# Performance work log

Hardware: AMD Instinct MI355X
Metric: run time of the kernel (lower is better)

Reference implementation:

```python
import jax, jax.numpy as jnp
import numpy as np

N_NODES = 100000
N_EDGES = 1600000
D_IN = 64
D_HID = 64
D_OUT = 64


def _sage_conv(x, src, dst, n_nodes, W_l, b_l, W_r):
    # mean aggregation of source features at destination nodes
    msgs = x[src]  # [E, F] gather
    agg = jax.ops.segment_sum(msgs, dst, num_segments=n_nodes)
    cnt = jax.ops.segment_sum(jnp.ones((src.shape[0],), x.dtype), dst, num_segments=n_nodes)
    mean = agg / jnp.maximum(cnt, 1.0)[:, None]  # nodes with no in-edges -> 0
    # out = lin_l(mean) + lin_r(x); lin_l has bias, lin_r does not (PyG default)
    return mean @ W_l.T + b_l + x @ W_r.T


def setup_inputs() -> dict:
    key = jax.random.key(0)
    ks = jax.random.split(key, 8)
    x = jax.random.normal(ks[0], (N_NODES, D_IN), dtype=jnp.float32)
    edge_index = jax.random.randint(ks[1], (2, N_EDGES), 0, N_NODES, dtype=jnp.int64) if jax.config.jax_enable_x64 else jax.random.randint(ks[1], (2, N_EDGES), 0, N_NODES, dtype=jnp.int32)
    s1 = 1.0 / np.sqrt(D_IN)
    s2 = 1.0 / np.sqrt(D_HID)
    W1_l = jax.random.uniform(ks[2], (D_HID, D_IN), jnp.float32, -s1, s1)
    b1_l = jax.random.uniform(ks[3], (D_HID,), jnp.float32, -s1, s1)
    W1_r = jax.random.uniform(ks[4], (D_HID, D_IN), jnp.float32, -s1, s1)
    W2_l = jax.random.uniform(ks[5], (D_OUT, D_HID), jnp.float32, -s2, s2)
    b2_l = jax.random.uniform(ks[6], (D_OUT,), jnp.float32, -s2, s2)
    W2_r = jax.random.uniform(ks[7], (D_OUT, D_HID), jnp.float32, -s2, s2)
    return {"x": x, "edge_index": edge_index, "W1_l": W1_l, "b1_l": b1_l, "W1_r": W1_r,
            "W2_l": W2_l, "b2_l": b2_l, "W2_r": W2_r}


def reference(x, edge_index, W1_l, b1_l, W1_r, W2_l, b2_l, W2_r):
    src, dst = edge_index[0], edge_index[1]
    h = _sage_conv(x, src, dst, x.shape[0], W1_l, b1_l, W1_r)
    h = jax.nn.relu(h)
    out = _sage_conv(h, src, dst, x.shape[0], W2_l, b2_l, W2_r)
    return out
```

## Files before the change

kernel.cpp:

```cpp
#include <hip/hip_runtime.h>
#include <hip/hip_fp16.h>

#define N_NODES 100000
#define N_EDGES 1600000
#define D 64

#define BSHIFT 7
#define BUCK_N 128
#define NBUCK 782
#define EPB 4096
#define NBLKA 391
#define SCAN_N (NBUCK * NBLKA)
#define SCAN_B1 ((SCAN_N + 255) / 256)
#define A4_CAP 3072
#define X_OCTETS (N_NODES * D / 8)
#define CVT_BLKS ((X_OCTETS + 2048 + 511) / 512)
#define AGB (N_NODES / 32)

typedef _Float16 half8 __attribute__((ext_vector_type(8)));
typedef float floatx4 __attribute__((ext_vector_type(4)));


__device__ __forceinline__ uint4 pack8h(float4 a, float4 b) {
    __half2 h0, h1, h2, h3;
    h0.x = __float2half(a.x); h0.y = __float2half(a.y);
    h1.x = __float2half(a.z); h1.y = __float2half(a.w);
    h2.x = __float2half(b.x); h2.y = __float2half(b.y);
    h3.x = __float2half(b.z); h3.y = __float2half(b.w);
    uint4 pk;
    pk.x = *(unsigned int*)&h0; pk.y = *(unsigned int*)&h1;
    pk.z = *(unsigned int*)&h2; pk.w = *(unsigned int*)&h3;
    return pk;
}


__global__ void pre_k(const float* __restrict__ x,
                      const float* __restrict__ W1l, const float* __restrict__ W1r,
                      const float* __restrict__ W2l, const float* __restrict__ W2r,
                      const int* __restrict__ dst, int* __restrict__ histG,
                      __half* __restrict__ x16,
                      __half* __restrict__ o1l, __half* __restrict__ o1r,
                      __half* __restrict__ o2l, __half* __restrict__ o2r) {
    __shared__ int hl[1024];
    int t = threadIdx.x;
    if (blockIdx.x < NBLKA) {
        hl[t] = 0; hl[t + 512] = 0;
        __syncthreads();
        int base = blockIdx.x * EPB;
#pragma unroll
        for (int r = 0; r < 8; r++) {
            int idx = base + r * 512 + t;
            if (idx < N_EDGES) atomicAdd(&hl[dst[idx] >> BSHIFT], 1);
        }
        __syncthreads();
        histG[t * NBLKA + blockIdx.x] = hl[t];
        int u = t + 512;
        if (u < NBUCK) histG[u * NBLKA + blockIdx.x] = hl[u];
        return;
    }
    int i = (blockIdx.x - NBLKA) * 512 + t;
    const float* s;
    __half* d;
    int j;
    if (i < X_OCTETS) {
        s = x; d = x16; j = i * 8;
    } else {
        int k = i - X_OCTETS;
        if (k >= 2048) return;
        int arr = k >> 9;
        j = (k & 511) * 8;
        s = (arr == 0) ? W1l : (arr == 1) ? W1r : (arr == 2) ? W2l : W2r;
        d = (arr == 0) ? o1l : (arr == 1) ? o1r : (arr == 2) ? o2l : o2r;
    }
    float4 a = *(const float4*)&s[j];
    float4 b = *(const float4*)&s[j + 4];
    *(uint4*)&d[j] = pack8h(a, b);
}


__global__ void scan1_k(int* __restrict__ data, int* __restrict__ bsums, int n) {
    __shared__ int sm[256];
    int i = blockIdx.x * 256 + threadIdx.x;
    int v = (i < n) ? data[i] : 0;
    sm[threadIdx.x] = v;
    __syncthreads();
    for (int off = 1; off < 256; off <<= 1) {
        int t = (threadIdx.x >= off) ? sm[threadIdx.x - off] : 0;
        __syncthreads();
        sm[threadIdx.x] += t;
        __syncthreads();
    }
    if (i < n) data[i] = sm[threadIdx.x] - v;
    if (threadIdx.x == 255) bsums[blockIdx.x] = sm[255];
}

__global__ void scan2_k(int* __restrict__ bsums, int nb) {
    __shared__ int sm[1024];
    int t = threadIdx.x;
    int i0 = 2 * t, i1 = 2 * t + 1;
    int v0 = (i0 < nb) ? bsums[i0] : 0;
    int v1 = (i1 < nb) ? bsums[i1] : 0;
    int p = v0 + v1;
    sm[t] = p;
    __syncthreads();
    for (int off = 1; off < 1024; off <<= 1) {
        int tt = (t >= off) ? sm[t - off] : 0;
        __syncthreads();
        sm[t] += tt;
        __syncthreads();
    }
    int S = sm[t];
    if (i0 < nb) bsums[i0] = S - v1;
    if (i1 < nb) bsums[i1] = S;
}

__device__ __forceinline__ int hist_abs(const int* histG, const int* bsums, int idx) {
    int v = histG[idx];
    int blk = idx >> 8;
    if (blk > 0) v += bsums[blk - 1];
    return v;
}


__global__ void a3_sort_k(const int* __restrict__ src, const int* __restrict__ dst,
                          const int* __restrict__ histG, const int* __restrict__ bsums,
                          unsigned int* __restrict__ epacked, int e) {
    __shared__ int hl[1024];
    __shared__ int cur[1024];
    __shared__ int sc[512];
    __shared__ int gbase[NBUCK];
    __shared__ unsigned int spk[EPB];
    __shared__ unsigned short sb[EPB];
    int t = threadIdx.x;
    int blk = blockIdx.x;
    int base = blk * EPB;

    hl[t] = 0; hl[t + 512] = 0;
    __syncthreads();

    int myd[8], mys[8];
#pragma unroll
    for (int r = 0; r < 8; r++) {
        int idx = base + r * 512 + t;
        if (idx < e) {
            myd[r] = dst[idx];
            mys[r] = src[idx];
            atomicAdd(&hl[myd[r] >> BSHIFT], 1);
        } else {
            myd[r] = -1; mys[r] = 0;
        }
    }
    __syncthreads();

    int v0 = hl[2 * t], v1 = hl[2 * t + 1];
    int p = v0 + v1;
    sc[t] = p;
    __syncthreads();
    for (int off = 1; off < 512; off <<= 1) {
        int tt = (t >= off) ? sc[t - off] : 0;
        __syncthreads();
        sc[t] += tt;
        __syncthreads();
    }
    int E = sc[t] - p;
    hl[2 * t] = E;       cur[2 * t] = E;
    hl[2 * t + 1] = E + v0; cur[2 * t + 1] = E + v0;
    if (t < NBUCK) gbase[t] = hist_abs(histG, bsums, t * NBLKA + blk);
    if (t + 512 < NBUCK) gbase[t + 512] = hist_abs(histG, bsums, (t + 512) * NBLKA + blk);
    __syncthreads();

#pragma unroll
    for (int r = 0; r < 8; r++) {
        if (myd[r] >= 0) {
            int b = myd[r] >> BSHIFT;
            int dl = myd[r] & (BUCK_N - 1);
            int pos = atomicAdd(&cur[b], 1);
            spk[pos] = ((unsigned)dl << 17) | (unsigned)mys[r];
            sb[pos] = (unsigned short)b;
        }
    }
    __syncthreads();

    int cnt = e - base; if (cnt > EPB) cnt = EPB;
#pragma unroll
    for (int r = 0; r < 8; r++) {
        int i = r * 512 + t;
        if (i < cnt) {
            int b = sb[i];
            epacked[gbase[b] + (i - hl[b])] = spk[i];
        }
    }
}


__global__ void a4_nodesort_k(unsigned int* __restrict__ epk,
                              const int* __restrict__ histG, const int* __restrict__ bsums,
                              int* __restrict__ row_ptr) {
    __shared__ int sorted[A4_CAP];
    __shared__ int hist[BUCK_N];
    __shared__ int cur[BUCK_N];
    __shared__ int sc[256];
    int b = blockIdx.x;
    int t = threadIdx.x;

    int s0 = hist_abs(histG, bsums, b * NBLKA);
    int s1 = (b == NBUCK - 1) ? N_EDGES : hist_abs(histG, bsums, (b + 1) * NBLKA);
    int cnt = s1 - s0;
    if (cnt > A4_CAP) cnt = A4_CAP;

    if (t < BUCK_N) hist[t] = 0;
    __syncthreads();

    unsigned int my[12];
    int mycnt = 0;
    for (int i = t; i < cnt; i += 256) {
        unsigned int p = epk[s0 + i];
        my[mycnt++] = p;
        atomicAdd(&hist[p >> 17], 1);
    }
    __syncthreads();

    int v = (t < BUCK_N) ? hist[t] : 0;
    sc[t] = v;
    __syncthreads();
    for (int off = 1; off < 256; off <<= 1) {
        int tt = (t >= off) ? sc[t - off] : 0;
        __syncthreads();
        sc[t] += tt;
        __syncthreads();
    }
    int start = sc[t] - v;
    if (t < BUCK_N) cur[t] = start;
    __syncthreads();

    for (int i = 0; i < mycnt; i++) {
        unsigned int p = my[i];
        int pos = atomicAdd(&cur[p >> 17], 1);
        sorted[pos] = (int)(p & 0x1FFFF);
    }
    __syncthreads();

    for (int i = t; i < cnt; i += 256) epk[s0 + i] = (unsigned int)sorted[i];

    if (t < BUCK_N) {
        int g = b * BUCK_N + t;
        if (g < N_NODES) row_ptr[g] = s0 + start;
    }
    if (b == NBUCK - 1 && t == 0) row_ptr[N_NODES] = N_EDGES;
}


__device__ __forceinline__ void addp(__half2* a, uint4 v) {
    const __half2* h = (const __half2*)&v;
    a[0] = __hadd2(a[0], h[0]);
    a[1] = __hadd2(a[1], h[1]);
    a[2] = __hadd2(a[2], h[2]);
    a[3] = __hadd2(a[3], h[3]);
}

__global__ void agg_gemm_k(const __half* __restrict__ feat16,
                           const int* __restrict__ row_ptr,
                           const int* __restrict__ adj,
                           const __half* __restrict__ Wl16,
                           const __half* __restrict__ Wr16,
                           const float* __restrict__ bl,
                           float* __restrict__ out32,
                           __half* __restrict__ out16,
                           int do_relu) {
    __shared__ __half mt[32 * 64];
    int t = threadIdx.x;
    int lane = t & 63;
    int w = t >> 6;
    int fp = lane & 7;
    int gl = lane & 56;
    int nloc = w * 8 + (lane >> 3);
    int node = blockIdx.x * 32 + nloc;
    const uint4* f16 = (const uint4*)feat16;

    int fcol = lane & 15;
    int quad = lane >> 4;
    int f = w * 16 + fcol;
    half8 b0 = *(const half8*)(Wl16 + (size_t)f * 64 + quad * 8);
    half8 b1 = *(const half8*)(Wl16 + (size_t)f * 64 + 32 + quad * 8);
    half8 b2 = *(const half8*)(Wr16 + (size_t)f * 64 + quad * 8);
    half8 b3 = *(const half8*)(Wr16 + (size_t)f * 64 + 32 + quad * 8);
    float bias = bl[f];

    int beg = row_ptr[node];
    int end = row_ptr[node + 1];
    __half2 z; z.x = __float2half(0.f); z.y = z.x;
    __half2 aA[4] = {z, z, z, z};
    __half2 aB[4] = {z, z, z, z};

    int e = beg;
    for (; e + 7 < end; e += 8) {
        int am = adj[e + fp];
        int n0 = __shfl(am, gl + 0);
        int n1 = __shfl(am, gl + 1);
        int n2 = __shfl(am, gl + 2);
        int n3 = __shfl(am, gl + 3);
        int n4 = __shfl(am, gl + 4);
        int n5 = __shfl(am, gl + 5);
        int n6 = __shfl(am, gl + 6);
        int n7 = __shfl(am, gl + 7);
        uint4 v0 = f16[(size_t)n0 * 8 + fp];
        uint4 v1 = f16[(size_t)n1 * 8 + fp];
        uint4 v2 = f16[(size_t)n2 * 8 + fp];
        uint4 v3 = f16[(size_t)n3 * 8 + fp];
        uint4 v4 = f16[(size_t)n4 * 8 + fp];
        uint4 v5 = f16[(size_t)n5 * 8 + fp];
        uint4 v6 = f16[(size_t)n6 * 8 + fp];
        uint4 v7 = f16[(size_t)n7 * 8 + fp];
        addp(aA, v0); addp(aB, v1); addp(aA, v2); addp(aB, v3);
        addp(aA, v4); addp(aB, v5); addp(aA, v6); addp(aB, v7);
    }
    if (e + 3 < end) {
        uint4 v0 = f16[(size_t)adj[e] * 8 + fp];
        uint4 v1 = f16[(size_t)adj[e + 1] * 8 + fp];
        uint4 v2 = f16[(size_t)adj[e + 2] * 8 + fp];
        uint4 v3 = f16[(size_t)adj[e + 3] * 8 + fp];
        addp(aA, v0); addp(aB, v1); addp(aA, v2); addp(aB, v3);
        e += 4;
    }
    for (; e < end; e++) addp(aA, f16[(size_t)adj[e] * 8 + fp]);

    int dg = end - beg;
    float inv = (dg > 1) ? 1.0f / (float)dg : 1.0f;
    float2 s0 = __half22float2(aA[0]), s1 = __half22float2(aA[1]);
    float2 s2 = __half22float2(aA[2]), s3 = __half22float2(aA[3]);
    float2 t0 = __half22float2(aB[0]), t1 = __half22float2(aB[1]);
    float2 t2 = __half22float2(aB[2]), t3 = __half22float2(aB[3]);
    float4 o0, o1;
    o0.x = (s0.x + t0.x) * inv; o0.y = (s0.y + t0.y) * inv;
    o0.z = (s1.x + t1.x) * inv; o0.w = (s1.y + t1.y) * inv;
    o1.x = (s2.x + t2.x) * inv; o1.y = (s2.y + t2.y) * inv;
    o1.z = (s3.x + t3.x) * inv; o1.w = (s3.y + t3.y) * inv;
    *(uint4*)&mt[(size_t)nloc * 64 + 8 * (fp ^ (nloc & 7))] = pack8h(o0, o1);
    __syncthreads();

#pragma unroll
    for (int tile = 0; tile < 2; tile++) {
        int row = tile * 16 + fcol;
        half8 a0 = *(const half8*)&mt[(size_t)row * 64 + 8 * (quad ^ (row & 7))];
        half8 a1 = *(const half8*)&mt[(size_t)row * 64 + 8 * ((4 + quad) ^ (row & 7))];
        size_t frow = ((size_t)blockIdx.x * 32 + row) * 64 + quad * 8;
        half8 a2 = *(const half8*)(feat16 + frow);
        half8 a3 = *(const half8*)(feat16 + frow + 32);

        floatx4 acc = {0.f, 0.f, 0.f, 0.f};
        acc = __builtin_amdgcn_mfma_f32_16x16x32_f16(a0, b0, acc, 0, 0, 0);
        acc = __builtin_amdgcn_mfma_f32_16x16x32_f16(a1, b1, acc, 0, 0, 0);
        acc = __builtin_amdgcn_mfma_f32_16x16x32_f16(a2, b2, acc, 0, 0, 0);
        acc = __builtin_amdgcn_mfma_f32_16x16x32_f16(a3, b3, acc, 0, 0, 0);

#pragma unroll
        for (int r = 0; r < 4; r++) {
            int node2 = blockIdx.x * 32 + tile * 16 + quad * 4 + r;
            float v = acc[r] + bias;
            if (do_relu) v = fmaxf(v, 0.f);
            if (out32) out32[(size_t)node2 * 64 + f] = v;
            if (out16) out16[(size_t)node2 * 64 + f] = __float2half(v);
        }
    }
}

extern "C" void kernel_launch(void* const* d_in, const int* in_sizes, int n_in,
                              void* d_out, int out_size, void* d_ws, size_t ws_size,
                              hipStream_t stream) {
    const float* x   = (const float*)d_in[0];
    const int*   ei  = (const int*)d_in[1];
    const float* W1l = (const float*)d_in[2];
    const float* b1l = (const float*)d_in[3];
    const float* W1r = (const float*)d_in[4];
    const float* W2l = (const float*)d_in[5];
    const float* b2l = (const float*)d_in[6];
    const float* W2r = (const float*)d_in[7];
    float* out = (float*)d_out;

    const int* src = ei;
    const int* dst = ei + N_EDGES;

    __half* x16   = (__half*)d_ws;
    __half* h16   = x16 + (size_t)N_NODES * D;
    __half* w1l16 = h16 + (size_t)N_NODES * D;
    __half* w1r16 = w1l16 + 4096;
    __half* w2l16 = w1r16 + 4096;
    __half* w2r16 = w2l16 + 4096;
    int*   histG = (int*)(w2r16 + 4096);
    int*   bsums = histG + SCAN_N;
    int*   row_ptr = bsums + 2048;
    unsigned int* epk = (unsigned int*)(row_ptr + N_NODES + 2);

    pre_k<<<NBLKA + CVT_BLKS, 512, 0, stream>>>(x, W1l, W1r, W2l, W2r, dst, histG,
                                                x16, w1l16, w1r16, w2l16, w2r16);

    scan1_k<<<SCAN_B1, 256, 0, stream>>>(histG, bsums, SCAN_N);
    scan2_k<<<1, 1024, 0, stream>>>(bsums, SCAN_B1);

    a3_sort_k<<<NBLKA, 512, 0, stream>>>(src, dst, histG, bsums, epk, N_EDGES);
    a4_nodesort_k<<<NBUCK, 256, 0, stream>>>(epk, histG, bsums, row_ptr);

    agg_gemm_k<<<AGB, 256, 0, stream>>>(x16, row_ptr, (const int*)epk,
                                        w1l16, w1r16, b1l,
                                        (float*)nullptr, h16, 1);
    agg_gemm_k<<<AGB, 256, 0, stream>>>(h16, row_ptr, (const int*)epk,
                                        w2l16, w2r16, b2l,
                                        out, (__half*)nullptr, 0);
}
```

Before: 199.6 us.

## Replace histogram+scan bucketing with atomic slot reservation into fixed-capacity buckets

Measured after the change: 201.2 us. About the same (+0.8%).

```diff
diff --git a/kernel.cpp b/kernel.cpp
--- a/kernel.cpp
+++ b/kernel.cpp
@@ -10,8 +10,6 @@
 #define NBUCK 782
 #define EPB 4096
 #define NBLKA 391
-#define SCAN_N (NBUCK * NBLKA)
-#define SCAN_B1 ((SCAN_N + 255) / 256)
 #define A4_CAP 3072
 #define X_OCTETS (N_NODES * D / 8)
 #define CVT_BLKS ((X_OCTETS + 2048 + 511) / 512)
@@ -34,106 +32,44 @@
 }
 
 
-__global__ void pre_k(const float* __restrict__ x,
-                      const float* __restrict__ W1l, const float* __restrict__ W1r,
-                      const float* __restrict__ W2l, const float* __restrict__ W2r,
-                      const int* __restrict__ dst, int* __restrict__ histG,
-                      __half* __restrict__ x16,
-                      __half* __restrict__ o1l, __half* __restrict__ o1r,
-                      __half* __restrict__ o2l, __half* __restrict__ o2r) {
-    __shared__ int hl[1024];
-    int t = threadIdx.x;
-    if (blockIdx.x < NBLKA) {
-        hl[t] = 0; hl[t + 512] = 0;
-        __syncthreads();
-        int base = blockIdx.x * EPB;
-#pragma unroll
-        for (int r = 0; r < 8; r++) {
-            int idx = base + r * 512 + t;
-            if (idx < N_EDGES) atomicAdd(&hl[dst[idx] >> BSHIFT], 1);
-        }
-        __syncthreads();
-        histG[t * NBLKA + blockIdx.x] = hl[t];
-        int u = t + 512;
-        if (u < NBUCK) histG[u * NBLKA + blockIdx.x] = hl[u];
-        return;
-    }
-    int i = (blockIdx.x - NBLKA) * 512 + t;
-    const float* s;
-    __half* d;
-    int j;
-    if (i < X_OCTETS) {
-        s = x; d = x16; j = i * 8;
-    } else {
-        int k = i - X_OCTETS;
-        if (k >= 2048) return;
-        int arr = k >> 9;
-        j = (k & 511) * 8;
-        s = (arr == 0) ? W1l : (arr == 1) ? W1r : (arr == 2) ? W2l : W2r;
-        d = (arr == 0) ? o1l : (arr == 1) ? o1r : (arr == 2) ? o2l : o2r;
-    }
-    float4 a = *(const float4*)&s[j];
-    float4 b = *(const float4*)&s[j + 4];
-    *(uint4*)&d[j] = pack8h(a, b);
-}
-
-
-__global__ void scan1_k(int* __restrict__ data, int* __restrict__ bsums, int n) {
-    __shared__ int sm[256];
-    int i = blockIdx.x * 256 + threadIdx.x;
-    int v = (i < n) ? data[i] : 0;
-    sm[threadIdx.x] = v;
-    __syncthreads();
-    for (int off = 1; off < 256; off <<= 1) {
-        int t = (threadIdx.x >= off) ? sm[threadIdx.x - off] : 0;
-        __syncthreads();
-        sm[threadIdx.x] += t;
-        __syncthreads();
-    }
-    if (i < n) data[i] = sm[threadIdx.x] - v;
-    if (threadIdx.x == 255) bsums[blockIdx.x] = sm[255];
-}
-
-__global__ void scan2_k(int* __restrict__ bsums, int nb) {
-    __shared__ int sm[1024];
-    int t = threadIdx.x;
-    int i0 = 2 * t, i1 = 2 * t + 1;
-    int v0 = (i0 < nb) ? bsums[i0] : 0;
-    int v1 = (i1 < nb) ? bsums[i1] : 0;
-    int p = v0 + v1;
-    sm[t] = p;
-    __syncthreads();
-    for (int off = 1; off < 1024; off <<= 1) {
-        int tt = (t >= off) ? sm[t - off] : 0;
-        __syncthreads();
-        sm[t] += tt;
-        __syncthreads();
-    }
-    int S = sm[t];
-    if (i0 < nb) bsums[i0] = S - v1;
-    if (i1 < nb) bsums[i1] = S;
-}
-
-__device__ __forceinline__ int hist_abs(const int* histG, const int* bsums, int idx) {
-    int v = histG[idx];
-    int blk = idx >> 8;
-    if (blk > 0) v += bsums[blk - 1];
-    return v;
-}
-
-
-__global__ void a3_sort_k(const int* __restrict__ src, const int* __restrict__ dst,
-                          const int* __restrict__ histG, const int* __restrict__ bsums,
-                          unsigned int* __restrict__ epacked, int e) {
+__global__ void build_k(const int* __restrict__ src, const int* __restrict__ dst,
+                        int* __restrict__ gcnt, unsigned int* __restrict__ epacked,
+                        const float* __restrict__ x,
+                        const float* __restrict__ W1l, const float* __restrict__ W1r,
+                        const float* __restrict__ W2l, const float* __restrict__ W2r,
+                        __half* __restrict__ x16,
+                        __half* __restrict__ o1l, __half* __restrict__ o1r,
+                        __half* __restrict__ o2l, __half* __restrict__ o2r) {
     __shared__ int hl[1024];
     __shared__ int cur[1024];
     __shared__ int sc[512];
-    __shared__ int gbase[NBUCK];
+    __shared__ int gbase[1024];
     __shared__ unsigned int spk[EPB];
     __shared__ unsigned short sb[EPB];
     int t = threadIdx.x;
-    int blk = blockIdx.x;
-    int base = blk * EPB;
+
+    if (blockIdx.x >= NBLKA) {
+        int i = (blockIdx.x - NBLKA) * 512 + t;
+        const float* s;
+        __half* d;
+        int j;
+        if (i < X_OCTETS) {
+            s = x; d = x16; j = i * 8;
+        } else {
+            int k = i - X_OCTETS;
+            if (k >= 2048) return;
+            int arr = k >> 9;
+            j = (k & 511) * 8;
+            s = (arr == 0) ? W1l : (arr == 1) ? W1r : (arr == 2) ? W2l : W2r;
+            d = (arr == 0) ? o1l : (arr == 1) ? o1r : (arr == 2) ? o2l : o2r;
+        }
+        float4 a = *(const float4*)&s[j];
+        float4 b = *(const float4*)&s[j + 4];
+        *(uint4*)&d[j] = pack8h(a, b);
+        return;
+    }
+
+    int base = blockIdx.x * EPB;
 
     hl[t] = 0; hl[t + 512] = 0;
     __syncthreads();
@@ -142,7 +78,7 @@
 #pragma unroll
     for (int r = 0; r < 8; r++) {
         int idx = base + r * 512 + t;
-        if (idx < e) {
+        if (idx < N_EDGES) {
             myd[r] = dst[idx];
             mys[r] = src[idx];
             atomicAdd(&hl[myd[r] >> BSHIFT], 1);
@@ -152,7 +88,10 @@
     }
     __syncthreads();
 
-    int v0 = hl[2 * t], v1 = hl[2 * t + 1];
+    int b0 = 2 * t, b1 = 2 * t + 1;
+    int v0 = hl[b0], v1 = hl[b1];
+    int r0 = (v0 > 0) ? atomicAdd(&gcnt[b0], v0) : 0;
+    int r1 = (v1 > 0) ? atomicAdd(&gcnt[b1], v1) : 0;
     int p = v0 + v1;
     sc[t] = p;
     __syncthreads();
@@ -163,10 +102,10 @@
         __syncthreads();
     }
     int E = sc[t] - p;
-    hl[2 * t] = E;       cur[2 * t] = E;
-    hl[2 * t + 1] = E + v0; cur[2 * t + 1] = E + v0;
-    if (t < NBUCK) gbase[t] = hist_abs(histG, bsums, t * NBLKA + blk);
-    if (t + 512 < NBUCK) gbase[t + 512] = hist_abs(histG, bsums, (t + 512) * NBLKA + blk);
+    hl[b0] = E;       cur[b0] = E;
+    hl[b1] = E + v0;  cur[b1] = E + v0;
+    gbase[b0] = b0 * A4_CAP + r0;
+    gbase[b1] = b1 * A4_CAP + r1;
     __syncthreads();
 
 #pragma unroll
@@ -181,7 +120,7 @@
     }
     __syncthreads();
 
-    int cnt = e - base; if (cnt > EPB) cnt = EPB;
+    int cnt = N_EDGES - base; if (cnt > EPB) cnt = EPB;
 #pragma unroll
     for (int r = 0; r < 8; r++) {
         int i = r * 512 + t;
@@ -194,8 +133,8 @@
 
 
 __global__ void a4_nodesort_k(unsigned int* __restrict__ epk,
-                              const int* __restrict__ histG, const int* __restrict__ bsums,
-                              int* __restrict__ row_ptr) {
+                              const int* __restrict__ gcnt,
+                              int* __restrict__ rbeg, int* __restrict__ rend) {
     __shared__ int sorted[A4_CAP];
     __shared__ int hist[BUCK_N];
     __shared__ int cur[BUCK_N];
@@ -203,9 +142,8 @@
     int b = blockIdx.x;
     int t = threadIdx.x;
 
-    int s0 = hist_abs(histG, bsums, b * NBLKA);
-    int s1 = (b == NBUCK - 1) ? N_EDGES : hist_abs(histG, bsums, (b + 1) * NBLKA);
-    int cnt = s1 - s0;
+    int s0 = b * A4_CAP;
+    int cnt = gcnt[b];
     if (cnt > A4_CAP) cnt = A4_CAP;
 
     if (t < BUCK_N) hist[t] = 0;
@@ -244,9 +182,11 @@
 
     if (t < BUCK_N) {
         int g = b * BUCK_N + t;
-        if (g < N_NODES) row_ptr[g] = s0 + start;
-    }
-    if (b == NBUCK - 1 && t == 0) row_ptr[N_NODES] = N_EDGES;
+        if (g < N_NODES) {
+            rbeg[g] = s0 + start;
+            rend[g] = s0 + start + v;
+        }
+    }
 }
 
 
@@ -259,7 +199,8 @@
 }
 
 __global__ void agg_gemm_k(const __half* __restrict__ feat16,
-                           const int* __restrict__ row_ptr,
+                           const int* __restrict__ rbeg,
+                           const int* __restrict__ rend,
                            const int* __restrict__ adj,
                            const __half* __restrict__ Wl16,
                            const __half* __restrict__ Wr16,
@@ -286,8 +227,8 @@
     half8 b3 = *(const half8*)(Wr16 + (size_t)f * 64 + 32 + quad * 8);
     float bias = bl[f];
 
-    int beg = row_ptr[node];
-    int end = row_ptr[node + 1];
+    int beg = rbeg[node];
+    int end = rend[node];
     __half2 z; z.x = __float2half(0.f); z.y = z.x;
     __half2 aA[4] = {z, z, z, z};
     __half2 aB[4] = {z, z, z, z};
@@ -386,24 +327,23 @@
     __half* w1r16 = w1l16 + 4096;
     __half* w2l16 = w1r16 + 4096;
     __half* w2r16 = w2l16 + 4096;
-    int*   histG = (int*)(w2r16 + 4096);
-    int*   bsums = histG + SCAN_N;
-    int*   row_ptr = bsums + 2048;
-    unsigned int* epk = (unsigned int*)(row_ptr + N_NODES + 2);
-
-    pre_k<<<NBLKA + CVT_BLKS, 512, 0, stream>>>(x, W1l, W1r, W2l, W2r, dst, histG,
-                                                x16, w1l16, w1r16, w2l16, w2r16);
-
-    scan1_k<<<SCAN_B1, 256, 0, stream>>>(histG, bsums, SCAN_N);
-    scan2_k<<<1, 1024, 0, stream>>>(bsums, SCAN_B1);
-
-    a3_sort_k<<<NBLKA, 512, 0, stream>>>(src, dst, histG, bsums, epk, N_EDGES);
-    a4_nodesort_k<<<NBUCK, 256, 0, stream>>>(epk, histG, bsums, row_ptr);
-
-    agg_gemm_k<<<AGB, 256, 0, stream>>>(x16, row_ptr, (const int*)epk,
+    int*   gcnt  = (int*)(w2r16 + 4096);
+    int*   rbeg  = gcnt + 1024;
+    int*   rend  = rbeg + N_NODES;
+    unsigned int* epk = (unsigned int*)(rend + N_NODES);
+
+    hipMemsetAsync(gcnt, 0, 1024 * sizeof(int), stream);
+
+    build_k<<<NBLKA + CVT_BLKS, 512, 0, stream>>>(src, dst, gcnt, epk,
+                                                  x, W1l, W1r, W2l, W2r,
+                                                  x16, w1l16, w1r16, w2l16, w2r16);
+
+    a4_nodesort_k<<<NBUCK, 256, 0, stream>>>(epk, gcnt, rbeg, rend);
+
+    agg_gemm_k<<<AGB, 256, 0, stream>>>(x16, rbeg, rend, (const int*)epk,
                                         w1l16, w1r16, b1l,
                                         (float*)nullptr, h16, 1);
-    agg_gemm_k<<<AGB, 256, 0, stream>>>(h16, row_ptr, (const int*)epk,
+    agg_gemm_k<<<AGB, 256, 0, stream>>>(h16, rbeg, rend, (const int*)epk,
                                         w2l16, w2r16, b2l,
                                         out, (__half*)nullptr, 0);
 }
```
